# Kernel tuning notes

Measured on AMD Instinct MI355X. Metric: run time of the kernel, lower is better.

## Reference

```python
import jax, jax.numpy as jnp
import numpy as np

HEAD = 8  # number of attention heads (init kwarg)


def setup_inputs() -> dict:
    key = jax.random.key(0)
    k1, k2, k3 = jax.random.split(key, 3)
    b, H, W, c = 8, 32, 32, 512
    dim = 512
    x = jax.random.normal(k1, (b, H, W, c), dtype=jnp.float32)
    # 1x1 Conv == per-pixel matmul over channels
    w_qkv = jax.random.normal(k2, (c, 3 * dim), dtype=jnp.float32) * (c ** -0.5)
    w_out = jax.random.normal(k3, (dim, dim), dtype=jnp.float32) * (dim ** -0.5)
    b_out = jnp.zeros((dim,), dtype=jnp.float32)
    return {"x": x, "w_qkv": w_qkv, "w_out": w_out, "b_out": b_out}


def reference(x, w_qkv, w_out, b_out):
    b, H, W, c = x.shape
    n = H * W
    # QKV 1x1-conv projection (no bias)
    qkv = jnp.einsum('bhwc,cd->bhwd', x, w_qkv)          # (b, H, W, 3*dim)
    qkv = qkv.reshape(b, n, HEAD, -1)                     # (b, n, head, 3*dh)
    q, k, v = jnp.split(qkv, 3, axis=-1)                  # each (b, n, head, dh)
    scale = b ** -0.5  # NOTE: source scales by batch size, reproduced faithfully
    attn = jax.nn.softmax(jnp.einsum('bihd,bjhd->bhij', q, k) * scale, axis=-1)
    out = jnp.einsum('bhij,bjhd->bihd', attn, v)          # (b, n, head, dh)
    out = out.reshape(b, H, W, -1)                        # (b, H, W, dim)
    # output 1x1-conv projection (with bias)
    return jnp.einsum('bhwc,cd->bhwd', out, w_out) + b_out
```

## Files before the change

kernel.cpp:

```cpp
#include <hip/hip_runtime.h>
#include <hip/hip_bf16.h>

typedef __bf16 bf16x8_t __attribute__((ext_vector_type(8)));
typedef float  f32x4_t  __attribute__((ext_vector_type(4)));
typedef short  s16x4_t  __attribute__((ext_vector_type(4)));
typedef short  s16x8_t  __attribute__((ext_vector_type(8)));

#define NTOK   1024
#define CDIM   512
#define QKVDIM 1536
#define NHEAD  8
#define DHEAD  64
#define C1EXP  0.51007088f
#define C2EXP  34.624681f

__device__ __forceinline__ float b2f(short s) {
    unsigned int u = ((unsigned int)(unsigned short)s) << 16;
    float f; __builtin_memcpy(&f, &u, 4); return f;
}
__device__ __forceinline__ short f2b(float f) {
    __bf16 h = (__bf16)f; short s; __builtin_memcpy(&s, &h, 2); return s;
}

__global__ __launch_bounds__(256) void cvt_fused(
    const float* __restrict__ x, const float* __restrict__ wq,
    short* __restrict__ xb, short* __restrict__ wqbT)
{
    int bid = blockIdx.x;
    if (bid < 2048) {
        int i = bid * 256 + threadIdx.x;
        const float* p = x + (size_t)i * 8;
        float4 a = *(const float4*)p, b = *(const float4*)(p + 4);
        s16x8_t v;
        v[0]=f2b(a.x); v[1]=f2b(a.y); v[2]=f2b(a.z); v[3]=f2b(a.w);
        v[4]=f2b(b.x); v[5]=f2b(b.y); v[6]=f2b(b.z); v[7]=f2b(b.w);
        *(s16x8_t*)(xb + (size_t)i * 8) = v;
    } else {
        int i = (bid - 2048) * 256 + threadIdx.x;
        int k = i / QKVDIM, n = i % QKVDIM;
        wqbT[(size_t)n * 512 + k] = f2b(wq[i]);
    }
}

__global__ __launch_bounds__(256) void cvtT(const float* __restrict__ in,
                                            short* __restrict__ out,
                                            int K, int N)
{
    int i = blockIdx.x * 256 + threadIdx.x;
    if (i < K * N) {
        int k = i / N, n = i % N;
        out[(size_t)n * K + k] = f2b(in[i]);
    }
}

__global__ __launch_bounds__(256) void gemm_qkv(
    const short* __restrict__ A, const short* __restrict__ Bt,
    short* __restrict__ qk, short* __restrict__ vT)
{
    constexpr int N = QKVDIM;
    __shared__ __align__(16) short Al[128 * 64];
    __shared__ __align__(16) short Bl[128 * 64];

    const int t = threadIdx.x;
    const int N0 = blockIdx.x * 128, M0 = blockIdx.y * 128;
    const int w = t >> 6, lane = t & 63;
    const int quad = lane >> 4, mr = lane & 15;
    const int wm = (w >> 1) * 64, wn = (w & 1) * 64;

    int srow[4], soff[4];
#pragma unroll
    for (int r = 0; r < 4; ++r) {
        int ci = r * 256 + t;
        srow[r] = ci >> 3;
        soff[r] = (ci & 7) * 8;
    }
    const short* Ag = A  + (size_t)M0 * 512;
    const short* Bg = Bt + (size_t)N0 * 512;

    s16x8_t ar[4], br[4];
#pragma unroll
    for (int r = 0; r < 4; ++r) {
        ar[r] = *(const s16x8_t*)(Ag + (size_t)srow[r] * 512 + soff[r]);
        br[r] = *(const s16x8_t*)(Bg + (size_t)srow[r] * 512 + soff[r]);
    }

    f32x4_t acc[4][4];
#pragma unroll
    for (int ms = 0; ms < 4; ++ms)
#pragma unroll
        for (int ns = 0; ns < 4; ++ns) acc[ms][ns] = f32x4_t{0.f,0.f,0.f,0.f};

#pragma unroll 1
    for (int kc = 0; kc < 8; ++kc) {
        __syncthreads();
#pragma unroll
        for (int r = 0; r < 4; ++r) {
            int lds = srow[r] * 64 + (((soff[r] >> 3) ^ (srow[r] & 7)) * 8);
            *(s16x8_t*)(Al + lds) = ar[r];
            *(s16x8_t*)(Bl + lds) = br[r];
        }
        __syncthreads();
        if (kc < 7) {
            int k0 = (kc + 1) * 64;
#pragma unroll
            for (int r = 0; r < 4; ++r) {
                ar[r] = *(const s16x8_t*)(Ag + (size_t)srow[r] * 512 + k0 + soff[r]);
                br[r] = *(const s16x8_t*)(Bg + (size_t)srow[r] * 512 + k0 + soff[r]);
            }
        }
#pragma unroll
        for (int kh = 0; kh < 2; ++kh) {
            bf16x8_t af[4], bf[4];
#pragma unroll
            for (int ms = 0; ms < 4; ++ms) {
                int rr = wm + ms * 16 + mr;
                af[ms] = *(const bf16x8_t*)(Al + rr * 64 + (((kh * 4 + quad) ^ (rr & 7)) * 8));
            }
#pragma unroll
            for (int ns = 0; ns < 4; ++ns) {
                int rr = wn + ns * 16 + mr;
                bf[ns] = *(const bf16x8_t*)(Bl + rr * 64 + (((kh * 4 + quad) ^ (rr & 7)) * 8));
            }
#pragma unroll
            for (int ms = 0; ms < 4; ++ms)
#pragma unroll
                for (int ns = 0; ns < 4; ++ns)
                    acc[ms][ns] = __builtin_amdgcn_mfma_f32_16x16x32_bf16(
                        af[ms], bf[ns], acc[ms][ns], 0, 0, 0);
        }
    }

#pragma unroll
    for (int ms = 0; ms < 4; ++ms) {
        int row = M0 + wm + ms * 16 + quad * 4;
        int bb = row >> 10, ti = row & 1023;
#pragma unroll
        for (int ns = 0; ns < 4; ++ns) {
            int c0 = N0 + wn + ns * 16;
            int hh = c0 / 192, r0 = c0 % 192;
            if (r0 < 128) {
                size_t base = (size_t)row * 1024 + hh * 128 + r0 + mr;
#pragma unroll
                for (int i = 0; i < 4; ++i)
                    qk[base + (size_t)i * 1024] = f2b(acc[ms][ns][i]);
            } else {
                s16x4_t v4;
#pragma unroll
                for (int i = 0; i < 4; ++i) v4[i] = f2b(acc[ms][ns][i]);
                *(s16x4_t*)(vT + ((size_t)(bb * 8 + hh) * 64 + (r0 - 128) + mr) * 1024 + ti) = v4;
            }
        }
    }
}

template <int N, bool BIAS, bool OUTF32>
__global__ __launch_bounds__(256) void gemm128(
    const short* __restrict__ A, const short* __restrict__ Bt,
    const float* __restrict__ bias, void* __restrict__ C)
{
    __shared__ __align__(16) short Al[128 * 64];
    __shared__ __align__(16) short Bl[128 * 64];

    const int t = threadIdx.x;
    const int N0 = blockIdx.x * 128, M0 = blockIdx.y * 128;
    const int w = t >> 6, lane = t & 63;
    const int quad = lane >> 4, mr = lane & 15;
    const int wm = (w >> 1) * 64, wn = (w & 1) * 64;

    int srow[4], soff[4];
#pragma unroll
    for (int r = 0; r < 4; ++r) {
        int ci = r * 256 + t;
        srow[r] = ci >> 3;
        soff[r] = (ci & 7) * 8;
    }
    const short* Ag = A  + (size_t)M0 * 512;
    const short* Bg = Bt + (size_t)N0 * 512;

    s16x8_t ar[4], br[4];
#pragma unroll
    for (int r = 0; r < 4; ++r) {
        ar[r] = *(const s16x8_t*)(Ag + (size_t)srow[r] * 512 + soff[r]);
        br[r] = *(const s16x8_t*)(Bg + (size_t)srow[r] * 512 + soff[r]);
    }

    f32x4_t acc[4][4];
#pragma unroll
    for (int ms = 0; ms < 4; ++ms)
#pragma unroll
        for (int ns = 0; ns < 4; ++ns) acc[ms][ns] = f32x4_t{0.f,0.f,0.f,0.f};

#pragma unroll 1
    for (int kc = 0; kc < 8; ++kc) {
        __syncthreads();
#pragma unroll
        for (int r = 0; r < 4; ++r) {
            int lds = srow[r] * 64 + (((soff[r] >> 3) ^ (srow[r] & 7)) * 8);
            *(s16x8_t*)(Al + lds) = ar[r];
            *(s16x8_t*)(Bl + lds) = br[r];
        }
        __syncthreads();
        if (kc < 7) {
            int k0 = (kc + 1) * 64;
#pragma unroll
            for (int r = 0; r < 4; ++r) {
                ar[r] = *(const s16x8_t*)(Ag + (size_t)srow[r] * 512 + k0 + soff[r]);
                br[r] = *(const s16x8_t*)(Bg + (size_t)srow[r] * 512 + k0 + soff[r]);
            }
        }
#pragma unroll
        for (int kh = 0; kh < 2; ++kh) {
            bf16x8_t af[4], bf[4];
#pragma unroll
            for (int ms = 0; ms < 4; ++ms) {
                int rr = wm + ms * 16 + mr;
                af[ms] = *(const bf16x8_t*)(Al + rr * 64 + (((kh * 4 + quad) ^ (rr & 7)) * 8));
            }
#pragma unroll
            for (int ns = 0; ns < 4; ++ns) {
                int rr = wn + ns * 16 + mr;
                bf[ns] = *(const bf16x8_t*)(Bl + rr * 64 + (((kh * 4 + quad) ^ (rr & 7)) * 8));
            }
#pragma unroll
            for (int ms = 0; ms < 4; ++ms)
#pragma unroll
                for (int ns = 0; ns < 4; ++ns)
                    acc[ms][ns] = __builtin_amdgcn_mfma_f32_16x16x32_bf16(
                        af[ms], bf[ns], acc[ms][ns], 0, 0, 0);
        }
    }

#pragma unroll
    for (int ms = 0; ms < 4; ++ms) {
        int row = M0 + wm + ms * 16 + quad * 4;
#pragma unroll
        for (int ns = 0; ns < 4; ++ns) {
            int col = N0 + wn + ns * 16 + mr;
            float bz = BIAS ? bias[col] : 0.f;
#pragma unroll
            for (int i = 0; i < 4; ++i) {
                if constexpr (OUTF32)
                    ((float*)C)[(size_t)(row + i) * N + col] = acc[ms][ns][i] + bz;
                else
                    ((short*)C)[(size_t)(row + i) * N + col] = f2b(acc[ms][ns][i]);
            }
        }
    }
}

__global__ __launch_bounds__(256) void attn_st(
    const short* __restrict__ qk, const short* __restrict__ vT,
    short* __restrict__ aout)
{
    __shared__ __align__(16) short Kl[64 * 72];
    __shared__ __align__(16) short Vt[64 * 72];
    __shared__ __align__(16) short Pl[4][16 * 72];

    const int t = threadIdx.x;
    const int g = blockIdx.x;
    const int qt = (g >> 3) & 15;
    const int bh = ((g >> 7) << 3) | (g & 7);
    const int h = bh & 7, b = bh >> 3;
    const int w = t >> 6, lane = t & 63;
    const int quad = lane >> 4, mr = lane & 15;

    const size_t qbase = (size_t)(b * NTOK + qt * 64 + w * 16 + mr) * 1024 + h * 128;
    const bf16x8_t qf0 = *(const bf16x8_t*)(qk + qbase + quad * 8);
    const bf16x8_t qf1 = *(const bf16x8_t*)(qk + qbase + 32 + quad * 8);

    float lsum = 0.f;
    f32x4_t O[4];
#pragma unroll
    for (int d = 0; d < 4; ++d) O[d] = f32x4_t{0.f, 0.f, 0.f, 0.f};

    short* Pm = Pl[w];

    const int r0i = t >> 3, r1i = r0i + 32, c8 = (t & 7) * 8;
    const size_t kgbase = (size_t)(b * NTOK) * 1024 + h * 128 + 64 + c8;
    const size_t vgbase = (size_t)(b * 8 + h) * 64 * 1024 + c8;

    s16x8_t k0r, k1r, v0r, v1r;
    k0r = *(const s16x8_t*)(qk + kgbase + (size_t)r0i * 1024);
    k1r = *(const s16x8_t*)(qk + kgbase + (size_t)r1i * 1024);
    v0r = *(const s16x8_t*)(vT + vgbase + (size_t)r0i * 1024);
    v1r = *(const s16x8_t*)(vT + vgbase + (size_t)r1i * 1024);

#pragma unroll 1
    for (int jt = 0; jt < 16; ++jt) {
        *(s16x8_t*)(Kl + r0i * 72 + c8) = k0r;
        *(s16x8_t*)(Kl + r1i * 72 + c8) = k1r;
        *(s16x8_t*)(Vt + r0i * 72 + c8) = v0r;
        *(s16x8_t*)(Vt + r1i * 72 + c8) = v1r;
        __syncthreads();

        if (jt < 15) {
            int j0n = (jt + 1) * 64;
            k0r = *(const s16x8_t*)(qk + kgbase + (size_t)(j0n + r0i) * 1024);
            k1r = *(const s16x8_t*)(qk + kgbase + (size_t)(j0n + r1i) * 1024);
            v0r = *(const s16x8_t*)(vT + vgbase + (size_t)r0i * 1024 + j0n);
            v1r = *(const s16x8_t*)(vT + vgbase + (size_t)r1i * 1024 + j0n);
        }

        f32x4_t s[4];
#pragma unroll
        for (int jj = 0; jj < 4; ++jj) {
            const short* kb = Kl + (jj * 16 + mr) * 72 + quad * 8;
            f32x4_t a0 = __builtin_amdgcn_mfma_f32_16x16x32_bf16(
                *(const bf16x8_t*)kb, qf0, f32x4_t{0.f,0.f,0.f,0.f}, 0, 0, 0);
            s[jj] = __builtin_amdgcn_mfma_f32_16x16x32_bf16(
                *(const bf16x8_t*)(kb + 32), qf1, a0, 0, 0, 0);
        }

#pragma unroll
        for (int jj = 0; jj < 4; ++jj) {
            s16x4_t pv;
#pragma unroll
            for (int r = 0; r < 4; ++r) {
                short hh = f2b(__builtin_amdgcn_exp2f(s[jj][r] * C1EXP - C2EXP));
                pv[r] = hh;
                lsum += b2f(hh);
            }
            *(s16x4_t*)(Pm + mr * 72 + jj * 16 + quad * 4) = pv;
        }

        bf16x8_t pa0 = *(const bf16x8_t*)(Pm + mr * 72 + quad * 8);
        bf16x8_t pa1 = *(const bf16x8_t*)(Pm + mr * 72 + 32 + quad * 8);

#pragma unroll
        for (int dt = 0; dt < 4; ++dt) {
            const short* vb = Vt + (dt * 16 + mr) * 72 + quad * 8;
            O[dt] = __builtin_amdgcn_mfma_f32_16x16x32_bf16(
                pa0, *(const bf16x8_t*)vb, O[dt], 0, 0, 0);
            O[dt] = __builtin_amdgcn_mfma_f32_16x16x32_bf16(
                pa1, *(const bf16x8_t*)(vb + 32), O[dt], 0, 0, 0);
        }
        __syncthreads();
    }

    lsum += __shfl_xor(lsum, 16, 64);
    lsum += __shfl_xor(lsum, 32, 64);
#pragma unroll
    for (int i = 0; i < 4; ++i) {
        float li = __shfl(lsum, quad * 4 + i, 64);
        float inv = 1.f / li;
        size_t tok = (size_t)(b * NTOK + qt * 64 + w * 16 + quad * 4 + i);
#pragma unroll
        for (int dt = 0; dt < 4; ++dt)
            aout[tok * CDIM + h * DHEAD + dt * 16 + mr] = f2b(O[dt][i] * inv);
    }
}

extern "C" void kernel_launch(void* const* d_in, const int* in_sizes, int n_in,
                              void* d_out, int out_size, void* d_ws, size_t ws_size,
                              hipStream_t stream)
{
    const float* x     = (const float*)d_in[0];
    const float* w_qkv = (const float*)d_in[1];
    const float* w_out = (const float*)d_in[2];
    const float* b_out = (const float*)d_in[3];
    for (int i = 0; i < n_in; ++i) {
        if      (in_sizes[i] == 4194304) x     = (const float*)d_in[i];
        else if (in_sizes[i] ==  786432) w_qkv = (const float*)d_in[i];
        else if (in_sizes[i] ==  262144) w_out = (const float*)d_in[i];
        else if (in_sizes[i] ==     512) b_out = (const float*)d_in[i];
    }

    short* qk   = (short*)d_ws;
    short* vT   = (short*)((char*)d_ws + (size_t)8192 * 1024 * 2);
    short* aout = (short*)((char*)d_ws + (size_t)8192 * 1024 * 2 + (size_t)64 * 64 * 1024 * 2);
    short* xb   = (short*)d_out;
    short* wqbT = (short*)d_out + (size_t)8192 * 512;
    short* wobT = (short*)d_ws;

    cvt_fused<<<5120, 256, 0, stream>>>(x, w_qkv, xb, wqbT);

    gemm_qkv<<<dim3(QKVDIM / 128, 8192 / 128), 256, 0, stream>>>(xb, wqbT, qk, vT);

    attn_st<<<1024, 256, 0, stream>>>(qk, vT, aout);

    cvtT<<<1024, 256, 0, stream>>>(w_out, wobT, 512, 512);

    gemm128<CDIM, true, true>
        <<<dim3(CDIM / 128, 8192 / 128), 256, 0, stream>>>(aout, wobT, b_out, d_out);
}
```

Before: 148.7 us.

## Load GEMM tiles directly into LDS and fold w_out conversion into cvt kernel

Both GEMM kernels now use global_load_lds (direct global-to-LDS 16-byte loads), with the XOR swizzle moved to the global address side, replacing register staging plus ds_write. The cvtT launch for w_out is merged into the fused conversion kernel, and wobT gets its own workspace region. The register prefetch of the next K-chunk is dropped, so global latency is no longer overlapped with MFMA work within a block, and the loop now relies on other resident blocks to hide it. One kernel launch is removed.

```diff
diff --git a/kernel.cpp b/kernel.cpp
--- a/kernel.cpp
+++ b/kernel.cpp
@@ -22,9 +22,16 @@
     __bf16 h = (__bf16)f; short s; __builtin_memcpy(&s, &h, 2); return s;
 }
 
+__device__ __forceinline__ void gload16(const void* g, void* l) {
+    __builtin_amdgcn_global_load_lds(
+        (const __attribute__((address_space(1))) void*)g,
+        (__attribute__((address_space(3))) void*)l, 16, 0, 0);
+}
+
 __global__ __launch_bounds__(256) void cvt_fused(
     const float* __restrict__ x, const float* __restrict__ wq,
-    short* __restrict__ xb, short* __restrict__ wqbT)
+    const float* __restrict__ wo, short* __restrict__ xb,
+    short* __restrict__ wqbT, short* __restrict__ wobT)
 {
     int bid = blockIdx.x;
     if (bid < 2048) {
@@ -35,21 +42,14 @@
         v[0]=f2b(a.x); v[1]=f2b(a.y); v[2]=f2b(a.z); v[3]=f2b(a.w);
         v[4]=f2b(b.x); v[5]=f2b(b.y); v[6]=f2b(b.z); v[7]=f2b(b.w);
         *(s16x8_t*)(xb + (size_t)i * 8) = v;
-    } else {
+    } else if (bid < 5120) {
         int i = (bid - 2048) * 256 + threadIdx.x;
         int k = i / QKVDIM, n = i % QKVDIM;
         wqbT[(size_t)n * 512 + k] = f2b(wq[i]);
-    }
-}
-
-__global__ __launch_bounds__(256) void cvtT(const float* __restrict__ in,
-                                            short* __restrict__ out,
-                                            int K, int N)
-{
-    int i = blockIdx.x * 256 + threadIdx.x;
-    if (i < K * N) {
-        int k = i / N, n = i % N;
-        out[(size_t)n * K + k] = f2b(in[i]);
+    } else {
+        int i = (bid - 5120) * 256 + threadIdx.x;
+        int k = i >> 9, n = i & 511;
+        wobT[(size_t)n * 512 + k] = f2b(wo[i]);
     }
 }
 
@@ -57,7 +57,6 @@
     const short* __restrict__ A, const short* __restrict__ Bt,
     short* __restrict__ qk, short* __restrict__ vT)
 {
-    constexpr int N = QKVDIM;
     __shared__ __align__(16) short Al[128 * 64];
     __shared__ __align__(16) short Bl[128 * 64];
 
@@ -67,23 +66,17 @@
     const int quad = lane >> 4, mr = lane & 15;
     const int wm = (w >> 1) * 64, wn = (w & 1) * 64;
 
-    int srow[4], soff[4];
+    int srow[4], goff[4], loff[4];
 #pragma unroll
     for (int r = 0; r < 4; ++r) {
         int ci = r * 256 + t;
         srow[r] = ci >> 3;
-        soff[r] = (ci & 7) * 8;
+        goff[r] = (((ci & 7) ^ (srow[r] & 7)) * 8);
+        loff[r] = ci * 8;
     }
     const short* Ag = A  + (size_t)M0 * 512;
     const short* Bg = Bt + (size_t)N0 * 512;
 
-    s16x8_t ar[4], br[4];
-#pragma unroll
-    for (int r = 0; r < 4; ++r) {
-        ar[r] = *(const s16x8_t*)(Ag + (size_t)srow[r] * 512 + soff[r]);
-        br[r] = *(const s16x8_t*)(Bg + (size_t)srow[r] * 512 + soff[r]);
-    }
-
     f32x4_t acc[4][4];
 #pragma unroll
     for (int ms = 0; ms < 4; ++ms)
@@ -93,21 +86,13 @@
 #pragma unroll 1
     for (int kc = 0; kc < 8; ++kc) {
         __syncthreads();
+        const int k0 = kc * 64;
 #pragma unroll
         for (int r = 0; r < 4; ++r) {
-            int lds = srow[r] * 64 + (((soff[r] >> 3) ^ (srow[r] & 7)) * 8);
-            *(s16x8_t*)(Al + lds) = ar[r];
-            *(s16x8_t*)(Bl + lds) = br[r];
-        }
-        __syncthreads();
-        if (kc < 7) {
-            int k0 = (kc + 1) * 64;
-#pragma unroll
-            for (int r = 0; r < 4; ++r) {
-                ar[r] = *(const s16x8_t*)(Ag + (size_t)srow[r] * 512 + k0 + soff[r]);
-                br[r] = *(const s16x8_t*)(Bg + (size_t)srow[r] * 512 + k0 + soff[r]);
-            }
-        }
+            gload16(Ag + (size_t)srow[r] * 512 + k0 + goff[r], Al + loff[r]);
+            gload16(Bg + (size_t)srow[r] * 512 + k0 + goff[r], Bl + loff[r]);
+        }
+        __syncthreads();
 #pragma unroll
         for (int kh = 0; kh < 2; ++kh) {
             bf16x8_t af[4], bf[4];
@@ -167,23 +152,17 @@
     const int quad = lane >> 4, mr = lane & 15;
     const int wm = (w >> 1) * 64, wn = (w & 1) * 64;
 
-    int srow[4], soff[4];
+    int srow[4], goff[4], loff[4];
 #pragma unroll
     for (int r = 0; r < 4; ++r) {
         int ci = r * 256 + t;
         srow[r] = ci >> 3;
-        soff[r] = (ci & 7) * 8;
+        goff[r] = (((ci & 7) ^ (srow[r] & 7)) * 8);
+        loff[r] = ci * 8;
     }
     const short* Ag = A  + (size_t)M0 * 512;
     const short* Bg = Bt + (size_t)N0 * 512;
 
-    s16x8_t ar[4], br[4];
-#pragma unroll
-    for (int r = 0; r < 4; ++r) {
-        ar[r] = *(const s16x8_t*)(Ag + (size_t)srow[r] * 512 + soff[r]);
-        br[r] = *(const s16x8_t*)(Bg + (size_t)srow[r] * 512 + soff[r]);
-    }
-
     f32x4_t acc[4][4];
 #pragma unroll
     for (int ms = 0; ms < 4; ++ms)
@@ -193,21 +172,13 @@
 #pragma unroll 1
     for (int kc = 0; kc < 8; ++kc) {
         __syncthreads();
+        const int k0 = kc * 64;
 #pragma unroll
         for (int r = 0; r < 4; ++r) {
-            int lds = srow[r] * 64 + (((soff[r] >> 3) ^ (srow[r] & 7)) * 8);
-            *(s16x8_t*)(Al + lds) = ar[r];
-            *(s16x8_t*)(Bl + lds) = br[r];
-        }
-        __syncthreads();
-        if (kc < 7) {
-            int k0 = (kc + 1) * 64;
-#pragma unroll
-            for (int r = 0; r < 4; ++r) {
-                ar[r] = *(const s16x8_t*)(Ag + (size_t)srow[r] * 512 + k0 + soff[r]);
-                br[r] = *(const s16x8_t*)(Bg + (size_t)srow[r] * 512 + k0 + soff[r]);
-            }
-        }
+            gload16(Ag + (size_t)srow[r] * 512 + k0 + goff[r], Al + loff[r]);
+            gload16(Bg + (size_t)srow[r] * 512 + k0 + goff[r], Bl + loff[r]);
+        }
+        __syncthreads();
 #pragma unroll
         for (int kh = 0; kh < 2; ++kh) {
             bf16x8_t af[4], bf[4];
@@ -368,17 +339,15 @@
     short* qk   = (short*)d_ws;
     short* vT   = (short*)((char*)d_ws + (size_t)8192 * 1024 * 2);
     short* aout = (short*)((char*)d_ws + (size_t)8192 * 1024 * 2 + (size_t)64 * 64 * 1024 * 2);
+    short* wobT = (short*)((char*)d_ws + (size_t)32 * 1024 * 1024 + (size_t)2 * 1024 * 1024);
     short* xb   = (short*)d_out;
     short* wqbT = (short*)d_out + (size_t)8192 * 512;
-    short* wobT = (short*)d_ws;
-
-    cvt_fused<<<5120, 256, 0, stream>>>(x, w_qkv, xb, wqbT);
+
+    cvt_fused<<<6144, 256, 0, stream>>>(x, w_qkv, w_out, xb, wqbT, wobT);
 
     gemm_qkv<<<dim3(QKVDIM / 128, 8192 / 128), 256, 0, stream>>>(xb, wqbT, qk, vT);
 
     attn_st<<<1024, 256, 0, stream>>>(qk, vT, aout);
-
-    cvtT<<<1024, 256, 0, stream>>>(w_out, wobT, 512, 512);
 
     gemm128<CDIM, true, true>
         <<<dim3(CDIM / 128, 8192 / 128), 256, 0, stream>>>(aout, wobT, b_out, d_out);
```

New measurement: 154.0 us. 3.6% more time.
